# Optimization experiments

Hardware: AMD Instinct MI355X
Metric: run time of the kernel (lower is better)

## Reference

```python
import jax, jax.numpy as jnp
import numpy as np

B, T, D, H, HD = 2, 2048, 1024, 16, 64


def setup_inputs() -> dict:
    key = jax.random.key(0)
    kx, kq, kk, kv, ko = jax.random.split(key, 5)
    s = 1.0 / np.sqrt(D)
    return {
        "x": jax.random.normal(kx, (B, T, D), dtype=jnp.float32),
        "Wq": jax.random.normal(kq, (H, D, HD), dtype=jnp.float32) * s,
        "Wk": jax.random.normal(kk, (H, D, HD), dtype=jnp.float32) * s,
        "Wv": jax.random.normal(kv, (H, D, HD), dtype=jnp.float32) * s,
        "Wo": jax.random.normal(ko, (D, D), dtype=jnp.float32) * s,
        "bo": jnp.zeros((D,), dtype=jnp.float32),
    }


def reference(x, Wq, Wk, Wv, Wo, bo):
    # Batched equivalent of the per-head loop: q/k/v for all heads at once.
    q = jnp.einsum("btd,hdk->bhtk", x, Wq)  # [B,H,T,HD]
    k = jnp.einsum("btd,hdk->bhtk", x, Wk)
    v = jnp.einsum("btd,hdk->bhtk", x, Wv)
    scale = 1.0 / jnp.sqrt(jnp.asarray(HD, dtype=x.dtype))
    scores = jnp.einsum("bhqk,bhsk->bhqs", q, k) * scale  # [B,H,T,T]
    causal = jnp.tril(jnp.ones((T, T), dtype=bool))
    scores = jnp.where(causal, scores, jnp.asarray(-1e9, dtype=scores.dtype))
    attn = jax.nn.softmax(scores, axis=-1)
    out = jnp.einsum("bhqs,bhsk->bhqk", attn, v)  # [B,H,T,HD]
    out = out.transpose(0, 2, 1, 3).reshape(B, T, H * HD)  # concat heads
    return out @ Wo + bo  # dropout is identity in eval (p used at train only)
```

## Files before the change

### kernel.cpp

```cpp
#include <hip/hip_runtime.h>
#include <hip/hip_bf16.h>
#include <stdint.h>
#include <stddef.h>

typedef __bf16 bf16_t;
typedef __attribute__((ext_vector_type(4))) __bf16 bf16x4;
typedef __attribute__((ext_vector_type(8))) __bf16 bf16x8;
typedef __attribute__((ext_vector_type(4))) float floatx4;

#define GLD16(gp, lp) __builtin_amdgcn_global_load_lds(                      \
    (__attribute__((address_space(1))) void*)(gp),                           \
    (__attribute__((address_space(3))) void*)(lp), 16, 0, 0)

__global__ __launch_bounds__(256) void prep(
    const float* __restrict__ x, const float* __restrict__ Wq,
    const float* __restrict__ Wk, const float* __restrict__ Wv,
    const float* __restrict__ Wo, bf16_t* __restrict__ XB,
    bf16_t* __restrict__ WT, bf16_t* __restrict__ WoT) {
  __shared__ bf16_t t[64][65];
  int bx = blockIdx.x;
  const int tid = threadIdx.x;
  if (bx < 2048) {
    const int i = (bx * 256 + tid) * 8;
    const float4 v0 = *(const float4*)(x + i);
    const float4 v1 = *(const float4*)(x + i + 4);
    bf16x8 o = {(bf16_t)v0.x, (bf16_t)v0.y, (bf16_t)v0.z, (bf16_t)v0.w,
                (bf16_t)v1.x, (bf16_t)v1.y, (bf16_t)v1.z, (bf16_t)v1.w};
    *(bf16x8*)(XB + i) = o;
    return;
  }
  bx -= 2048;
  const int g = tid >> 6, l = tid & 63;
  if (bx < 768) {
    const int d0 = (bx & 15) * 64, h = (bx >> 4) & 15, z = bx >> 8;
    const float* W = (z == 0) ? Wq : (z == 1) ? Wk : Wv;
    const float scl = (z == 0) ? 0.18033688011112042f : 1.0f;
    const float* src = W + (size_t)h * 65536 + (size_t)d0 * 64;
    #pragma unroll
    for (int i = 0; i < 16; ++i) { int r = g * 16 + i; t[r][l] = (bf16_t)(src[(size_t)r * 64 + l] * scl); }
    __syncthreads();
    bf16_t* dst = WT + ((size_t)z * 1024 + h * 64) * 1024 + d0;
    #pragma unroll
    for (int i = 0; i < 16; ++i) { int c = g * 16 + i; dst[(size_t)c * 1024 + l] = t[l][c]; }
  } else {
    bx -= 768;
    const int r0 = (bx & 15) * 64, c0 = (bx >> 4) * 64;
    #pragma unroll
    for (int i = 0; i < 16; ++i) { int r = g * 16 + i; t[r][l] = (bf16_t)Wo[(size_t)(r0 + r) * 1024 + c0 + l]; }
    __syncthreads();
    #pragma unroll
    for (int i = 0; i < 16; ++i) { int c = g * 16 + i; WoT[(size_t)(c0 + c) * 1024 + r0 + l] = t[l][c]; }
  }
}

template <bool BIAS, typename OutT, int NT>
__device__ __forceinline__ void gemm_body(
    const bf16_t* __restrict__ A, const bf16_t* __restrict__ Bt,
    OutT* __restrict__ C, const float* __restrict__ bias,
    int K, int lda, int ldb, int ldc, int m0, int n0,
    bf16_t* As, bf16_t* Bs) {
  const int tid = threadIdx.x;
  const int lane = tid & 63, w = tid >> 6;
  const int qd = lane >> 4, ln = lane & 15;
  const int wm = (w & 1) * 64, wn = (w >> 1) * (NT * 16);

  const floatx4 z4 = {0.f, 0.f, 0.f, 0.f};
  floatx4 acc[4][NT];
  #pragma unroll
  for (int i = 0; i < 4; ++i)
    #pragma unroll
    for (int j = 0; j < NT; ++j) acc[i][j] = z4;

  for (int k0 = 0; k0 < K; k0 += 64) {
    #pragma unroll
    for (int i = 0; i < 4; ++i) {
      const int c = tid + i * 256;
      const int row = c >> 3;
      const int sg = (c & 7) ^ (row & 7);
      GLD16(A + (size_t)(m0 + row) * lda + k0 + sg * 8, As + (size_t)(w * 64 + i * 256) * 8);
    }
    #pragma unroll
    for (int i = 0; i < NT; ++i) {
      const int c = tid + i * 256;
      const int row = c >> 3;
      const int sg = (c & 7) ^ (row & 7);
      GLD16(Bt + (size_t)(n0 + row) * ldb + k0 + sg * 8, Bs + (size_t)(w * 64 + i * 256) * 8);
    }
    __syncthreads();
    #pragma unroll
    for (int h = 0; h < 2; ++h) {
      bf16x8 af[4], bfr[NT];
      #pragma unroll
      for (int t = 0; t < 4; ++t) {
        const int ra = wm + t * 16 + ln;
        af[t]  = *(const bf16x8*)(As + (size_t)ra * 64 + (((h * 4 + qd) ^ (ra & 7)) * 8));
      }
      #pragma unroll
      for (int t = 0; t < NT; ++t) {
        const int rb = wn + t * 16 + ln;
        bfr[t] = *(const bf16x8*)(Bs + (size_t)rb * 64 + (((h * 4 + qd) ^ (rb & 7)) * 8));
      }
      #pragma unroll
      for (int mt = 0; mt < 4; ++mt)
        #pragma unroll
        for (int nt = 0; nt < NT; ++nt)
          acc[mt][nt] = __builtin_amdgcn_mfma_f32_16x16x32_bf16(af[mt], bfr[nt], acc[mt][nt], 0, 0, 0);
    }
    __syncthreads();
  }

  #pragma unroll
  for (int nt = 0; nt < NT; ++nt) {
    const int col = n0 + wn + nt * 16 + ln;
    const float bv = BIAS ? bias[col] : 0.f;
    #pragma unroll
    for (int mt = 0; mt < 4; ++mt) {
      const int row = m0 + wm + mt * 16 + qd * 4;
      #pragma unroll
      for (int r = 0; r < 4; ++r)
        C[(size_t)(row + r) * ldc + col] = (OutT)(acc[mt][nt][r] + bv);
    }
  }
}

__global__ __launch_bounds__(256) void proj_gemm(
    const bf16_t* __restrict__ XB, const bf16_t* __restrict__ WT,
    bf16_t* __restrict__ C1, bf16_t* __restrict__ VT) {
  __shared__ __align__(16) bf16_t As[128 * 64];
  __shared__ __align__(16) bf16_t Bs[128 * 64];
  int bx = blockIdx.x;
  if (bx < 512) {
    gemm_body<false, bf16_t, 4>(XB, WT, C1, nullptr, 1024, 1024, 1024, 2048,
                                (bx & 31) * 128, (bx >> 5) * 128, As, Bs);
  } else {
    bx -= 512;
    gemm_body<false, bf16_t, 4>(WT + (size_t)2048 * 1024, XB, VT, nullptr,
                                1024, 1024, 1024, 4096,
                                (bx & 7) * 128, (bx >> 3) * 128, As, Bs);
  }
}

__global__ __launch_bounds__(256) void out_gemm(
    const bf16_t* __restrict__ AO, const bf16_t* __restrict__ WoT,
    float* __restrict__ C, const float* __restrict__ bias) {
  __shared__ __align__(16) bf16_t As[128 * 64];
  __shared__ __align__(16) bf16_t Bs[64 * 64];
  gemm_body<true, float, 2>(AO, WoT, C, bias, 1024, 1024, 1024, 1024,
                            blockIdx.x * 128, blockIdx.y * 64, As, Bs);
}

__global__ __launch_bounds__(256, 4) void flash_attn(
    const bf16_t* __restrict__ C1, const bf16_t* __restrict__ VT,
    bf16_t* __restrict__ AO) {
  __shared__ __align__(16) bf16_t Ks[2][64 * 64];
  __shared__ __align__(16) bf16_t Vs[2][64 * 64];
  __shared__ __align__(16) bf16_t Ps[4][16 * 64];

  const int bid = blockIdx.x;
  const int g = bid & 31;
  const int b = g >> 4, h = g & 15;
  const int v = bid >> 5, j = v & 7, sel = v >> 3;
  const int qt = (sel == 0) ? j : (sel == 1) ? 15 - j : (sel == 2) ? 16 + j : 31 - j;

  const int tid = threadIdx.x, lane = tid & 63, w = tid >> 6;
  const int qd = lane >> 4, ln = lane & 15;
  const bf16_t* Qb = C1 + (size_t)b * 2048 * 2048;

  bf16x8 qf0, qf1;
  {
    const bf16_t* qp = Qb + (size_t)(qt * 64 + w * 16 + ln) * 2048 + h * 64 + qd * 8;
    qf0 = *(const bf16x8*)qp;
    qf1 = *(const bf16x8*)(qp + 32);
  }
  const floatx4 z4 = {0.f, 0.f, 0.f, 0.f};
  floatx4 oacc[4];
  #pragma unroll
  for (int t = 0; t < 4; ++t) oacc[t] = z4;
  floatx4 osum = z4;
  const bf16_t one = (bf16_t)1.0f;
  const bf16x8 vone = {one, one, one, one, one, one, one, one};

  const bf16_t* Kg = Qb + 1024 + h * 64;
  const bf16_t* Vg = VT + (size_t)(h * 64) * 4096 + b * 2048;

  const int r0 = tid >> 3;
  const int g0 = ((tid & 7) ^ (r0 & 7)) * 8;

  auto STAGE = [&](int BUF, int SOFF) {
    GLD16(Kg + (size_t)(SOFF + r0) * 2048 + g0,      &Ks[BUF][w * 512]);
    GLD16(Kg + (size_t)(SOFF + r0 + 32) * 2048 + g0, &Ks[BUF][w * 512 + 2048]);
    GLD16(Vg + (size_t)r0 * 4096 + SOFF + g0,        &Vs[BUF][w * 512]);
    GLD16(Vg + (size_t)(r0 + 32) * 4096 + SOFF + g0, &Vs[BUF][w * 512 + 2048]);
  };

  STAGE(0, 0);

  const int e2 = (ln & 7) << 1;
  const int swf = qd ^ (ln & 7);

  for (int st = 0; st <= qt; ++st) {
    const int bi = st & 1;
    __syncthreads();
    if (st < qt) STAGE(bi ^ 1, (st + 1) * 64);

    floatx4 sa[4];
    __builtin_amdgcn_s_setprio(1);
    #pragma unroll
    for (int nt = 0; nt < 4; ++nt) {
      const bf16_t* kp = &Ks[bi][(nt * 16 + ln) * 64];
      bf16x8 kf0 = *(const bf16x8*)(kp + swf * 8);
      bf16x8 kf1 = *(const bf16x8*)(kp + (swf ^ 4) * 8);
      floatx4 t0 = z4;
      t0 = __builtin_amdgcn_mfma_f32_16x16x32_bf16(kf0, qf0, t0, 0, 0, 0);
      t0 = __builtin_amdgcn_mfma_f32_16x16x32_bf16(kf1, qf1, t0, 0, 0, 0);
      sa[nt] = t0;
    }
    __builtin_amdgcn_s_setprio(0);

    bf16x8 vf0[4], vf1[4];
    #pragma unroll
    for (int t = 0; t < 4; ++t) {
      const bf16_t* vp = &Vs[bi][(t * 16 + ln) * 64];
      vf0[t] = *(const bf16x8*)(vp + swf * 8);
      vf1[t] = *(const bf16x8*)(vp + (swf ^ 4) * 8);
    }

    #pragma unroll
    for (int nt = 0; nt < 4; ++nt) {
      float p[4];
      #pragma unroll
      for (int r = 0; r < 4; ++r) {
        float v2 = sa[nt][r];
        if (st == qt && (nt * 16 + qd * 4 + r) > (w * 16 + ln)) v2 = -1e30f;
        p[r] = __builtin_amdgcn_exp2f(v2);
      }
      bf16x4 pk = {(bf16_t)p[0], (bf16_t)p[1], (bf16_t)p[2], (bf16_t)p[3]};
      *(bf16x4*)(&Ps[w][ln * 64 + (((nt * 4 + qd) ^ e2) << 2)]) = pk;
    }
    bf16x8 pa0 = *(const bf16x8*)(&Ps[w][ln * 64 + ((((qd << 1)    ) ^ e2) << 2)]);
    bf16x8 pa1 = *(const bf16x8*)(&Ps[w][ln * 64 + ((((qd << 1) + 8) ^ e2) << 2)]);

    __builtin_amdgcn_s_setprio(1);
    #pragma unroll
    for (int t = 0; t < 4; ++t) {
      oacc[t] = __builtin_amdgcn_mfma_f32_16x16x32_bf16(pa0, vf0[t], oacc[t], 0, 0, 0);
      oacc[t] = __builtin_amdgcn_mfma_f32_16x16x32_bf16(pa1, vf1[t], oacc[t], 0, 0, 0);
    }
    osum = __builtin_amdgcn_mfma_f32_16x16x32_bf16(pa0, vone, osum, 0, 0, 0);
    osum = __builtin_amdgcn_mfma_f32_16x16x32_bf16(pa1, vone, osum, 0, 0, 0);
    __builtin_amdgcn_s_setprio(0);
  }

  #pragma unroll
  for (int r = 0; r < 4; ++r) {
    const float lr = 1.0f / osum[r];
    #pragma unroll
    for (int t = 0; t < 4; ++t) {
      const int col = h * 64 + t * 16 + ln;
      const int row = b * 2048 + qt * 64 + w * 16 + qd * 4 + r;
      AO[(size_t)row * 1024 + col] = (bf16_t)(oacc[t][r] * lr);
    }
  }
}

extern "C" void kernel_launch(void* const* d_in, const int* in_sizes, int n_in,
                              void* d_out, int out_size, void* d_ws, size_t ws_size,
                              hipStream_t stream) {
  const float* x  = (const float*)d_in[0];
  const float* Wq = (const float*)d_in[1];
  const float* Wk = (const float*)d_in[2];
  const float* Wv = (const float*)d_in[3];
  const float* Wo = (const float*)d_in[4];
  const float* bo = (const float*)d_in[5];
  float* out = (float*)d_out;

  bf16_t* WT  = (bf16_t*)d_ws;
  bf16_t* WoT = WT + (size_t)3072 * 1024;
  bf16_t* C1  = WoT + (size_t)1024 * 1024;
  bf16_t* AO  = C1 + (size_t)4096 * 2048;
  bf16_t* XB  = (bf16_t*)d_out;
  bf16_t* VT  = XB + (size_t)4096 * 1024;

  prep<<<dim3(3072), 256, 0, stream>>>(x, Wq, Wk, Wv, Wo, XB, WT, WoT);
  proj_gemm<<<dim3(768), 256, 0, stream>>>(XB, WT, C1, VT);
  flash_attn<<<dim3(1024), 256, 0, stream>>>(C1, VT, AO);
  out_gemm<<<dim3(32, 16), 256, 0, stream>>>(AO, WoT, out, bo);
}
```

Baseline: 166.6 us.

## Switch flash attention to 32x32x16 MFMA with register-shuffled P operand

Rewrites the attention kernel to use 32x32x16 bf16 MFMA tiles, with 2 waves per block each covering 32 query rows instead of 4 waves of 16 rows. The softmax probabilities are repacked into the A-operand layout in registers through cross-half lane shuffles, which removes the per-wave LDS round trip for P. This cuts LDS traffic and instruction count per tile. In exchange it halves threads per block, so each thread issues twice as many K/V staging loads, and it raises register pressure with 16-wide accumulators.

```diff
diff --git a/kernel.cpp b/kernel.cpp
--- a/kernel.cpp
+++ b/kernel.cpp
@@ -4,9 +4,12 @@
 #include <stddef.h>
 
 typedef __bf16 bf16_t;
+typedef __attribute__((ext_vector_type(2))) __bf16 bf16x2;
 typedef __attribute__((ext_vector_type(4))) __bf16 bf16x4;
 typedef __attribute__((ext_vector_type(8))) __bf16 bf16x8;
 typedef __attribute__((ext_vector_type(4))) float floatx4;
+typedef __attribute__((ext_vector_type(16))) float floatx16;
+typedef __attribute__((ext_vector_type(4))) int intx4;
 
 #define GLD16(gp, lp) __builtin_amdgcn_global_load_lds(                      \
     (__attribute__((address_space(1))) void*)(gp),                           \
@@ -149,12 +152,16 @@
                             blockIdx.x * 128, blockIdx.y * 64, As, Bs);
 }
 
-__global__ __launch_bounds__(256, 4) void flash_attn(
+__device__ __forceinline__ int pk2(float lo, float hi) {
+  bf16x2 t; t[0] = (bf16_t)lo; t[1] = (bf16_t)hi;
+  return __builtin_bit_cast(int, t);
+}
+
+__global__ __launch_bounds__(128, 2) void flash_attn(
     const bf16_t* __restrict__ C1, const bf16_t* __restrict__ VT,
     bf16_t* __restrict__ AO) {
   __shared__ __align__(16) bf16_t Ks[2][64 * 64];
   __shared__ __align__(16) bf16_t Vs[2][64 * 64];
-  __shared__ __align__(16) bf16_t Ps[4][16 * 64];
 
   const int bid = blockIdx.x;
   const int g = bid & 31;
@@ -163,20 +170,20 @@
   const int qt = (sel == 0) ? j : (sel == 1) ? 15 - j : (sel == 2) ? 16 + j : 31 - j;
 
   const int tid = threadIdx.x, lane = tid & 63, w = tid >> 6;
-  const int qd = lane >> 4, ln = lane & 15;
+  const int r32 = lane & 31, hh = lane >> 5;
   const bf16_t* Qb = C1 + (size_t)b * 2048 * 2048;
 
-  bf16x8 qf0, qf1;
+  bf16x8 qf[4];
   {
-    const bf16_t* qp = Qb + (size_t)(qt * 64 + w * 16 + ln) * 2048 + h * 64 + qd * 8;
-    qf0 = *(const bf16x8*)qp;
-    qf1 = *(const bf16x8*)(qp + 32);
-  }
-  const floatx4 z4 = {0.f, 0.f, 0.f, 0.f};
-  floatx4 oacc[4];
+    const bf16_t* qp = Qb + (size_t)(qt * 64 + w * 32 + r32) * 2048 + h * 64 + hh * 8;
+    #pragma unroll
+    for (int c = 0; c < 4; ++c) qf[c] = *(const bf16x8*)(qp + c * 16);
+  }
+
+  floatx16 z16;
   #pragma unroll
-  for (int t = 0; t < 4; ++t) oacc[t] = z4;
-  floatx4 osum = z4;
+  for (int i = 0; i < 16; ++i) z16[i] = 0.f;
+  floatx16 oacc0 = z16, oacc1 = z16, osum = z16;
   const bf16_t one = (bf16_t)1.0f;
   const bf16x8 vone = {one, one, one, one, one, one, one, one};
 
@@ -187,79 +194,91 @@
   const int g0 = ((tid & 7) ^ (r0 & 7)) * 8;
 
   auto STAGE = [&](int BUF, int SOFF) {
-    GLD16(Kg + (size_t)(SOFF + r0) * 2048 + g0,      &Ks[BUF][w * 512]);
-    GLD16(Kg + (size_t)(SOFF + r0 + 32) * 2048 + g0, &Ks[BUF][w * 512 + 2048]);
-    GLD16(Vg + (size_t)r0 * 4096 + SOFF + g0,        &Vs[BUF][w * 512]);
-    GLD16(Vg + (size_t)(r0 + 32) * 4096 + SOFF + g0, &Vs[BUF][w * 512 + 2048]);
+    #pragma unroll
+    for (int k = 0; k < 4; ++k)
+      GLD16(Kg + (size_t)(SOFF + r0 + 16 * k) * 2048 + g0, &Ks[BUF][w * 512 + k * 1024]);
+    #pragma unroll
+    for (int k = 0; k < 4; ++k)
+      GLD16(Vg + (size_t)(r0 + 16 * k) * 4096 + SOFF + g0, &Vs[BUF][w * 512 + k * 1024]);
   };
 
   STAGE(0, 0);
 
-  const int e2 = (ln & 7) << 1;
-  const int swf = qd ^ (ln & 7);
+  const int fk = r32 & 7;
 
   for (int st = 0; st <= qt; ++st) {
     const int bi = st & 1;
     __syncthreads();
     if (st < qt) STAGE(bi ^ 1, (st + 1) * 64);
 
-    floatx4 sa[4];
+    floatx16 p0 = z16, p1 = z16;
     __builtin_amdgcn_s_setprio(1);
     #pragma unroll
-    for (int nt = 0; nt < 4; ++nt) {
-      const bf16_t* kp = &Ks[bi][(nt * 16 + ln) * 64];
-      bf16x8 kf0 = *(const bf16x8*)(kp + swf * 8);
-      bf16x8 kf1 = *(const bf16x8*)(kp + (swf ^ 4) * 8);
-      floatx4 t0 = z4;
-      t0 = __builtin_amdgcn_mfma_f32_16x16x32_bf16(kf0, qf0, t0, 0, 0, 0);
-      t0 = __builtin_amdgcn_mfma_f32_16x16x32_bf16(kf1, qf1, t0, 0, 0, 0);
-      sa[nt] = t0;
+    for (int c = 0; c < 4; ++c) {
+      const int sl = ((2 * c + hh) ^ fk) * 8;
+      bf16x8 kf0 = *(const bf16x8*)(&Ks[bi][r32 * 64 + sl]);
+      bf16x8 kf1 = *(const bf16x8*)(&Ks[bi][(32 + r32) * 64 + sl]);
+      p0 = __builtin_amdgcn_mfma_f32_32x32x16_bf16(kf0, qf[c], p0, 0, 0, 0);
+      p1 = __builtin_amdgcn_mfma_f32_32x32x16_bf16(kf1, qf[c], p1, 0, 0, 0);
     }
     __builtin_amdgcn_s_setprio(0);
 
-    bf16x8 vf0[4], vf1[4];
-    #pragma unroll
-    for (int t = 0; t < 4; ++t) {
-      const bf16_t* vp = &Vs[bi][(t * 16 + ln) * 64];
-      vf0[t] = *(const bf16x8*)(vp + swf * 8);
-      vf1[t] = *(const bf16x8*)(vp + (swf ^ 4) * 8);
-    }
-
-    #pragma unroll
-    for (int nt = 0; nt < 4; ++nt) {
-      float p[4];
-      #pragma unroll
-      for (int r = 0; r < 4; ++r) {
-        float v2 = sa[nt][r];
-        if (st == qt && (nt * 16 + qd * 4 + r) > (w * 16 + ln)) v2 = -1e30f;
-        p[r] = __builtin_amdgcn_exp2f(v2);
+    const int qloc = w * 32 + r32;
+    #pragma unroll
+    for (int reg = 0; reg < 16; ++reg) {
+      const int srow = (reg & 3) + 8 * (reg >> 2) + 4 * hh;
+      float a = p0[reg], c2 = p1[reg];
+      if (st == qt) {
+        if (srow > qloc) a = -1e30f;
+        if (32 + srow > qloc) c2 = -1e30f;
       }
-      bf16x4 pk = {(bf16_t)p[0], (bf16_t)p[1], (bf16_t)p[2], (bf16_t)p[3]};
-      *(bf16x4*)(&Ps[w][ln * 64 + (((nt * 4 + qd) ^ e2) << 2)]) = pk;
-    }
-    bf16x8 pa0 = *(const bf16x8*)(&Ps[w][ln * 64 + ((((qd << 1)    ) ^ e2) << 2)]);
-    bf16x8 pa1 = *(const bf16x8*)(&Ps[w][ln * 64 + ((((qd << 1) + 8) ^ e2) << 2)]);
+      p0[reg] = __builtin_amdgcn_exp2f(a);
+      p1[reg] = __builtin_amdgcn_exp2f(c2);
+    }
+
+    bf16x8 pa[4];
+    {
+      auto MKPA = [&](const floatx16& e, bf16x8& A8, bf16x8& B8) {
+        int u0 = pk2(e[0], e[1]),  u1 = pk2(e[2], e[3]);
+        int u2 = pk2(e[4], e[5]),  u3 = pk2(e[6], e[7]);
+        int u4 = pk2(e[8], e[9]),  u5 = pk2(e[10], e[11]);
+        int u6 = pk2(e[12], e[13]), u7 = pk2(e[14], e[15]);
+        int s0 = __shfl_xor(hh ? u0 : u2, 32);
+        int s1 = __shfl_xor(hh ? u1 : u3, 32);
+        int s2 = __shfl_xor(hh ? u4 : u6, 32);
+        int s3 = __shfl_xor(hh ? u5 : u7, 32);
+        intx4 A, B;
+        A[0] = hh ? s0 : u0;  A[1] = hh ? s1 : u1;
+        A[2] = hh ? u2 : s0;  A[3] = hh ? u3 : s1;
+        B[0] = hh ? s2 : u4;  B[1] = hh ? s3 : u5;
+        B[2] = hh ? u6 : s2;  B[3] = hh ? u7 : s3;
+        A8 = __builtin_bit_cast(bf16x8, A);
+        B8 = __builtin_bit_cast(bf16x8, B);
+      };
+      MKPA(p0, pa[0], pa[1]);
+      MKPA(p1, pa[2], pa[3]);
+    }
 
     __builtin_amdgcn_s_setprio(1);
     #pragma unroll
-    for (int t = 0; t < 4; ++t) {
-      oacc[t] = __builtin_amdgcn_mfma_f32_16x16x32_bf16(pa0, vf0[t], oacc[t], 0, 0, 0);
-      oacc[t] = __builtin_amdgcn_mfma_f32_16x16x32_bf16(pa1, vf1[t], oacc[t], 0, 0, 0);
-    }
-    osum = __builtin_amdgcn_mfma_f32_16x16x32_bf16(pa0, vone, osum, 0, 0, 0);
-    osum = __builtin_amdgcn_mfma_f32_16x16x32_bf16(pa1, vone, osum, 0, 0, 0);
+    for (int c = 0; c < 4; ++c) {
+      const int sl = ((2 * c + hh) ^ fk) * 8;
+      bf16x8 vf0 = *(const bf16x8*)(&Vs[bi][r32 * 64 + sl]);
+      bf16x8 vf1 = *(const bf16x8*)(&Vs[bi][(32 + r32) * 64 + sl]);
+      oacc0 = __builtin_amdgcn_mfma_f32_32x32x16_bf16(pa[c], vf0, oacc0, 0, 0, 0);
+      oacc1 = __builtin_amdgcn_mfma_f32_32x32x16_bf16(pa[c], vf1, oacc1, 0, 0, 0);
+      osum  = __builtin_amdgcn_mfma_f32_32x32x16_bf16(pa[c], vone, osum, 0, 0, 0);
+    }
     __builtin_amdgcn_s_setprio(0);
   }
 
   #pragma unroll
-  for (int r = 0; r < 4; ++r) {
-    const float lr = 1.0f / osum[r];
-    #pragma unroll
-    for (int t = 0; t < 4; ++t) {
-      const int col = h * 64 + t * 16 + ln;
-      const int row = b * 2048 + qt * 64 + w * 16 + qd * 4 + r;
-      AO[(size_t)row * 1024 + col] = (bf16_t)(oacc[t][r] * lr);
-    }
+  for (int reg = 0; reg < 16; ++reg) {
+    const float lr = 1.0f / osum[reg];
+    const int qrow = (reg & 3) + 8 * (reg >> 2) + 4 * hh;
+    const size_t row = (size_t)(b * 2048 + qt * 64 + w * 32 + qrow);
+    AO[row * 1024 + h * 64 + r32]      = (bf16_t)(oacc0[reg] * lr);
+    AO[row * 1024 + h * 64 + 32 + r32] = (bf16_t)(oacc1[reg] * lr);
   }
 }
 
@@ -283,6 +302,6 @@
 
   prep<<<dim3(3072), 256, 0, stream>>>(x, Wq, Wk, Wv, Wo, XB, WT, WoT);
   proj_gemm<<<dim3(768), 256, 0, stream>>>(XB, WT, C1, VT);
-  flash_attn<<<dim3(1024), 256, 0, stream>>>(C1, VT, AO);
+  flash_attn<<<dim3(1024), 128, 0, stream>>>(C1, VT, AO);
   out_gemm<<<dim3(32, 16), 256, 0, stream>>>(AO, WoT, out, bo);
 }
```

New measurement: 176.0 us. 1.06x slower.
